# Optimization experiments

Hardware: AMD Instinct MI355X
Metric: run time of the kernel (lower is better)

The kernel has to match this reference:

```python
import jax, jax.numpy as jnp
import numpy as np

B = 4          # graphs
N = 8192       # coarse nodes (2048/graph)
M = 65536      # fine (skip) nodes (16384/graph)
E = 131072     # edges (32768/graph)
T = 16         # global tokens per graph
F_IN = 16      # dim of x and x_skip (concat -> in_channels = 32)
HID, OUT = 32, 16
ED, GD, EMB, H = 3, 1024, 64, 4
K = 3


def _make_pe(t, d):
    # PositionalEncoding buffer (sin/cos), deterministic constant
    position = np.arange(t, dtype=np.float32)[:, None]
    div = np.exp(np.arange(0, d, 2, dtype=np.float32) * (-np.log(10000.0) / d))
    pe = np.zeros((t, d), dtype=np.float32)
    pe[:, 0::2] = np.sin(position * div)
    pe[:, 1::2] = np.cos(position * div)
    return jnp.asarray(pe)


def setup_inputs():
    key = jax.random.key(0)
    ks = jax.random.split(key, 30)
    n, m, e = N // B, M // B, E // B
    inp = {}
    inp['x'] = jax.random.normal(ks[0], (N, F_IN), jnp.float32)
    inp['pos'] = jax.random.normal(ks[1], (N, 3), jnp.float32)
    inp['batch'] = jnp.repeat(jnp.arange(B), n)
    inp['x_skip'] = jax.random.normal(ks[2], (M, F_IN), jnp.float32)
    inp['pos_skip'] = jax.random.normal(ks[3], (M, 3), jnp.float32)
    inp['batch_skip'] = jnp.repeat(jnp.arange(B), m)
    off = jnp.repeat(jnp.arange(B) * m, e)
    inp['edge_index'] = jax.random.randint(ks[4], (2, E), 0, m) + off[None, :]
    inp['global_token'] = jax.random.normal(ks[5], (B * T, GD), jnp.float32)
    def lin(k, o, i, s):
        return jax.random.normal(k, (o, i), jnp.float32) * s
    inp['Wq_w'] = lin(ks[6], EMB, ED, 0.3); inp['Wq_b'] = jnp.zeros((EMB,), jnp.float32)
    inp['Wk_w'] = lin(ks[7], EMB, GD, 0.03); inp['Wk_b'] = jnp.zeros((EMB,), jnp.float32)
    inp['Wv_w'] = lin(ks[8], EMB, GD, 0.03); inp['Wv_b'] = jnp.zeros((EMB,), jnp.float32)
    inp['in_proj_w'] = lin(ks[9], 3 * EMB, EMB, 0.125); inp['in_proj_b'] = jnp.zeros((3 * EMB,), jnp.float32)
    inp['out_w'] = lin(ks[10], EMB, EMB, 0.125); inp['out_b'] = jnp.zeros((EMB,), jnp.float32)
    dims = [(2 * F_IN, HID), (HID, HID), (HID, OUT)]
    for i, (ci, co) in enumerate(dims):
        inp[f'nn_w{i}'] = lin(ks[11 + 3 * i], ci * co, ED + EMB, 0.05)
        inp[f'nn_b{i}'] = jnp.zeros((ci * co,), jnp.float32)
        inp[f'root{i}'] = jax.random.normal(ks[12 + 3 * i], (ci, co), jnp.float32) * (1.0 / np.sqrt(ci))
        inp[f'bias{i}'] = jnp.zeros((co,), jnp.float32)
    return inp


def reference(x, pos, batch, x_skip, pos_skip, batch_skip, edge_index, global_token,
              Wq_w, Wq_b, Wk_w, Wk_b, Wv_w, Wv_b, in_proj_w, in_proj_b, out_w, out_b,
              nn_w0, nn_b0, root0, bias0, nn_w1, nn_b1, root1, bias1, nn_w2, nn_b2, root2, bias2):
    # ---- knn_interpolate (k=3, inverse squared-distance weighting) ----
    # graphs are equal-sized by construction so per-graph knn == batched knn
    pos_b = pos.reshape(B, -1, 3)
    posk_b = pos_skip.reshape(B, -1, 3)
    d2 = ((posk_b ** 2).sum(-1)[:, :, None] + (pos_b ** 2).sum(-1)[:, None, :]
          - 2.0 * jnp.einsum('bmc,bnc->bmn', posk_b, pos_b))  # [B,m,n]
    neg, idx = jax.lax.top_k(-d2, K)                           # [B,m,K]
    w = 1.0 / jnp.maximum(-neg, 1e-16)
    x_b = x.reshape(B, -1, x.shape[-1])
    feats = jnp.take_along_axis(x_b[:, None, :, :], idx[:, :, :, None], axis=2)  # [B,m,K,F]
    xf = ((w[..., None] * feats).sum(2) / w.sum(2)[..., None]).reshape(M, -1)

    src, dst = edge_index[0], edge_index[1]
    pseudo = pos_skip[dst] - pos_skip[src]                     # patch_size is None
    edge_pos = (0.5 * (pos_skip[dst] + pos_skip[src])).reshape(B, -1, 3)
    gt = global_token.reshape(B, -1, global_token.shape[-1])
    pe = _make_pe(gt.shape[1], EMB)
    Q = edge_pos @ Wq_w.T + Wq_b                               # [B,Eb,EMB]
    Kt = gt @ Wk_w.T + Wk_b + pe                               # dropout in eval = identity
    Vt = gt @ Wv_w.T + Wv_b + pe
    # ---- MultiheadAttention (batch_first) ----
    wq, wk, wv = jnp.split(in_proj_w, 3, axis=0)
    bq, bk, bv = jnp.split(in_proj_b, 3, axis=0)
    hd = EMB // H
    def heads(t, w_, b_):
        t = t @ w_.T + b_
        return t.reshape(t.shape[0], t.shape[1], H, hd).transpose(0, 2, 1, 3)
    q, k_, v = heads(Q, wq, bq), heads(Kt, wk, bk), heads(Vt, wv, bv)
    att = jax.nn.softmax(jnp.einsum('bhqd,bhkd->bhqk', q, k_) / np.sqrt(hd).astype(np.float32), axis=-1)
    o = jnp.einsum('bhqk,bhkd->bhqd', att, v).transpose(0, 2, 1, 3).reshape(B, -1, EMB)
    o = o @ out_w.T + out_b
    pseudo = jnp.concatenate([pseudo, o.reshape(-1, EMB)], axis=-1)  # [E, 3+64]

    # ---- NNConv stack (gather -> edge MLP -> per-edge matmul -> scatter mean) ----
    h = jnp.concatenate([xf, x_skip], axis=1)                  # [M, 32]
    ones = jnp.ones((E,), jnp.float32)
    cnt = jnp.maximum(jax.ops.segment_sum(ones, dst, num_segments=M), 1.0)[:, None]
    for nw, nb, rt, bs in ((nn_w0, nn_b0, root0, bias0),
                           (nn_w1, nn_b1, root1, bias1),
                           (nn_w2, nn_b2, root2, bias2)):
        ci, co = rt.shape
        we = jax.nn.relu(pseudo @ nw.T + nb).reshape(E, ci, co)  # MLP (BN at default eval stats ~ identity)
        msg = jnp.einsum('ei,eio->eo', h[src], we)               # [E, co]
        aggr = jax.ops.segment_sum(msg, dst, num_segments=M) / cnt
        h = jax.nn.relu(aggr + h @ rt + bs)                      # drop_act=False -> relu every layer
    return h, pos_skip, batch_skip
```

## Files before the change

kernel.cpp:

```cpp
#include <hip/hip_runtime.h>
#include <math.h>

#define NB    4
#define NN    8192
#define MM    65536
#define EE    131072
#define NPG   2048

typedef short short8 __attribute__((ext_vector_type(8)));
typedef float f32x4  __attribute__((ext_vector_type(4)));

static __device__ inline unsigned short f2b(float f) {
    unsigned u = __float_as_uint(f);
    u += 0x7fffu + ((u >> 16) & 1u);
    return (unsigned short)(u >> 16);
}
static __device__ inline unsigned f2b_pack(float a, float b) {
    unsigned x = __float_as_uint(a); x += 0x7fffu + ((x >> 16) & 1u);
    unsigned y = __float_as_uint(b); y += 0x7fffu + ((y >> 16) & 1u);
    return (x >> 16) | (y & 0xffff0000u);
}
static __device__ inline short8 bc8(uint4 v) {
    union { uint4 u; short8 s; } c; c.u = v; return c.s;
}

__global__ __launch_bounds__(256)
void k_knn(const float* __restrict__ pos, const float* __restrict__ pos_skip,
           const float* __restrict__ x, const float* __restrict__ x_skip,
           const int* __restrict__ batch_skip,
           float* __restrict__ h0, float* __restrict__ out_pos,
           float* __restrict__ out_batch)
{
    __shared__ float4 cp[NPG];
    __shared__ unsigned pk[4][128][3];
    __shared__ float wFin[128][3];
    __shared__ int   iFin[128][3];

    int tid = threadIdx.x;
    int g = blockIdx.x >> 7;
    int cbase = g * NPG;
    for (int c = tid; c < NPG; c += 256) {
        float px = pos[(cbase + c) * 3 + 0];
        float py = pos[(cbase + c) * 3 + 1];
        float pz = pos[(cbase + c) * 3 + 2];
        cp[c] = make_float4(px, py, pz, px * px + py * py + pz * pz);
    }
    __syncthreads();

    int p = tid & 63;
    int slice = tid >> 6;
    int fbase = blockIdx.x * 128;
    int f0 = fbase + p, f1 = fbase + 64 + p;
    float fx0 = pos_skip[f0 * 3 + 0], fy0 = pos_skip[f0 * 3 + 1], fz0 = pos_skip[f0 * 3 + 2];
    float fx1 = pos_skip[f1 * 3 + 0], fy1 = pos_skip[f1 * 3 + 1], fz1 = pos_skip[f1 * 3 + 2];
    float fq0 = fx0 * fx0 + fy0 * fy0 + fz0 * fz0;
    float fq1 = fx1 * fx1 + fy1 * fy1 + fz1 * fz1;

    unsigned ka0 = 0xFFFFFFFFu, ka1 = 0xFFFFFFFFu, ka2 = 0xFFFFFFFFu;
    unsigned kb0 = 0xFFFFFFFFu, kb1 = 0xFFFFFFFFu, kb2 = 0xFFFFFFFFu;
    const float4* cps = cp + slice * 512;
#pragma unroll 8
    for (int l = 0; l < 512; ++l) {
        float4 cc = cps[l];
        float s0 = fx0 * cc.x + fy0 * cc.y + fz0 * cc.z;
        float d0 = fmaxf(fq0 + cc.w - 2.f * s0, 0.f);
        unsigned k = (__float_as_uint(d0) & 0xFFFFFE00u) | (unsigned)l;
        unsigned t1 = max(ka0, k); ka0 = min(ka0, k);
        unsigned t2 = max(ka1, t1); ka1 = min(ka1, t1);
        ka2 = min(ka2, t2);
        float s1 = fx1 * cc.x + fy1 * cc.y + fz1 * cc.z;
        float d1 = fmaxf(fq1 + cc.w - 2.f * s1, 0.f);
        unsigned kq = (__float_as_uint(d1) & 0xFFFFFE00u) | (unsigned)l;
        t1 = max(kb0, kq); kb0 = min(kb0, kq);
        t2 = max(kb1, t1); kb1 = min(kb1, t1);
        kb2 = min(kb2, t2);
    }
    pk[slice][p][0] = ka0; pk[slice][p][1] = ka1; pk[slice][p][2] = ka2;
    pk[slice][64 + p][0] = kb0; pk[slice][64 + p][1] = kb1; pk[slice][64 + p][2] = kb2;
    __syncthreads();

    if (tid < 128) {
        int n = tid;
        int f = fbase + n;
        float gx = pos_skip[f * 3 + 0], gy = pos_skip[f * 3 + 1], gz = pos_skip[f * 3 + 2];
        float gq = gx * gx + gy * gy + gz * gz;
        unsigned long long m0 = ~0ull, m1 = ~0ull, m2 = ~0ull;
#pragma unroll
        for (int s = 0; s < 4; ++s)
#pragma unroll
            for (int r = 0; r < 3; ++r) {
                unsigned key = pk[s][n][r];
                int c = s * 512 + (int)(key & 511u);
                float4 cc = cp[c];
                float d = fmaxf(gq + cc.w - 2.f * (gx * cc.x + gy * cc.y + gz * cc.z), 0.f);
                unsigned long long kk = ((unsigned long long)__float_as_uint(d) << 32) | (unsigned)c;
                unsigned long long t1 = m0 > kk ? m0 : kk; m0 = m0 < kk ? m0 : kk;
                unsigned long long t2 = m1 > t1 ? m1 : t1; m1 = m1 < t1 ? m1 : t1;
                m2 = m2 < t2 ? m2 : t2;
            }
        float d0 = __uint_as_float((unsigned)(m0 >> 32));
        float d1 = __uint_as_float((unsigned)(m1 >> 32));
        float d2 = __uint_as_float((unsigned)(m2 >> 32));
        float w0 = 1.f / fmaxf(d0, 1e-16f);
        float w1 = 1.f / fmaxf(d1, 1e-16f);
        float w2 = 1.f / fmaxf(d2, 1e-16f);
        float inv = 1.f / (w0 + w1 + w2);
        wFin[n][0] = w0 * inv; wFin[n][1] = w1 * inv; wFin[n][2] = w2 * inv;
        iFin[n][0] = cbase + (int)(m0 & 2047u);
        iFin[n][1] = cbase + (int)(m1 & 2047u);
        iFin[n][2] = cbase + (int)(m2 & 2047u);
        out_pos[f * 3 + 0] = gx; out_pos[f * 3 + 1] = gy; out_pos[f * 3 + 2] = gz;
        out_batch[f] = (float)batch_skip[f];
    }
    __syncthreads();

    int n2 = tid >> 1, half = tid & 1;
    int f2 = fbase + n2;
    float4* h04 = (float4*)(h0 + (size_t)f2 * 32);
    if (half == 0) {
        const float4* x4 = (const float4*)x;
        float w0 = wFin[n2][0], w1 = wFin[n2][1], w2 = wFin[n2][2];
        int a0 = iFin[n2][0] * 4, a1 = iFin[n2][1] * 4, a2 = iFin[n2][2] * 4;
#pragma unroll
        for (int j = 0; j < 4; ++j) {
            float4 v0 = x4[a0 + j], v1 = x4[a1 + j], v2 = x4[a2 + j];
            float4 r;
            r.x = w0 * v0.x + w1 * v1.x + w2 * v2.x;
            r.y = w0 * v0.y + w1 * v1.y + w2 * v2.y;
            r.z = w0 * v0.z + w1 * v1.z + w2 * v2.z;
            r.w = w0 * v0.w + w1 * v1.w + w2 * v2.w;
            h04[j] = r;
        }
    } else {
        const float4* xs4 = (const float4*)x_skip;
#pragma unroll
        for (int j = 0; j < 4; ++j) h04[4 + j] = xs4[f2 * 4 + j];
    }
}

__global__ __launch_bounds__(128)
void k_tokens1(const float* __restrict__ gt,
               const float* __restrict__ Wk_w, const float* __restrict__ Wk_b,
               const float* __restrict__ Wv_w, const float* __restrict__ Wv_b,
               float* __restrict__ KtVt)
{
    int b = blockIdx.x >> 4;
    int t = blockIdx.x & 15;
    int which = threadIdx.x >> 6;
    int d = threadIdx.x & 63;
    const float* W = which ? Wv_w : Wk_w;
    const float* bias = which ? Wv_b : Wk_b;
    const float4* row = (const float4*)(gt + (size_t)(b * 16 + t) * 1024);
    const float4* wr = (const float4*)(W + (size_t)d * 1024);
    float acc = 0.f;
    for (int c = 0; c < 256; ++c) {
        float4 a = row[c], w = wr[c];
        acc += a.x * w.x; acc += a.y * w.y; acc += a.z * w.z; acc += a.w * w.w;
    }
    int i2 = d >> 1;
    float dv = expf((float)(2 * i2) * (-0.14391156831212787f));
    float ang = (float)t * dv;
    float pe = (d & 1) ? cosf(ang) : sinf(ang);
    KtVt[((size_t)(b * 2 + which) * 16 + t) * 64 + d] = acc + bias[d] + pe;
}

__global__ __launch_bounds__(256)
void k_tokens2(const float* __restrict__ KtVt,
               const float* __restrict__ in_proj_w, const float* __restrict__ in_proj_b,
               const float* __restrict__ out_w,
               const float* __restrict__ Wq_w, const float* __restrict__ Wq_b,
               float* __restrict__ Mfold, uint4* __restrict__ v2fG)
{
    int b = blockIdx.x;
    int tid = threadIdx.x;
    __shared__ float KtL[1024], VtL[1024], vv[1024], kproj[1024];
    __shared__ float v2L[4096];
    __shared__ float qWs[192], qbs[64];
    for (int idx = tid; idx < 1024; idx += 256) {
        KtL[idx] = KtVt[(size_t)(b * 2 + 0) * 1024 + idx];
        VtL[idx] = KtVt[(size_t)(b * 2 + 1) * 1024 + idx];
    }
    __syncthreads();
    for (int idx = tid; idx < 2048; idx += 256) {
        int which = idx >> 10; int td = idx & 1023; int t = td >> 6; int j = td & 63;
        int r = (which ? 128 : 64) + j;
        const float* w = in_proj_w + (size_t)r * 64;
        const float* src = which ? VtL : KtL;
        float acc = in_proj_b[r];
#pragma unroll 8
        for (int dd = 0; dd < 64; ++dd) acc += src[t * 64 + dd] * w[dd];
        if (which) vv[t * 64 + j] = acc;
        else kproj[t * 64 + j] = acc;
    }
    for (int idx = tid; idx < 192; idx += 256) {
        int c = idx >> 6; int j = idx & 63;
        float acc = 0.f;
        for (int dd = 0; dd < 64; ++dd) acc += in_proj_w[(size_t)j * 64 + dd] * Wq_w[dd * 3 + c];
        qWs[c * 64 + j] = acc;
    }
    for (int j = tid; j < 64; j += 256) {
        float acc = in_proj_b[j];
        for (int dd = 0; dd < 64; ++dd) acc += in_proj_w[(size_t)j * 64 + dd] * Wq_b[dd];
        qbs[j] = acc;
    }
    __syncthreads();
    for (int idx = tid; idx < 4096; idx += 256) {
        int jo = idx & 63; int th2 = idx >> 6; int h = th2 & 3; int t = th2 >> 2;
        float acc = 0.f;
#pragma unroll
        for (int dd = 0; dd < 16; ++dd)
            acc += vv[t * 64 + h * 16 + dd] * out_w[(size_t)jo * 64 + h * 16 + dd];
        v2L[(t * 4 + h) * 64 + jo] = acc;
    }
    {
        int th = tid >> 2, c = tid & 3;
        int t = th >> 2, h = th & 3;
        float acc = 0.f;
#pragma unroll
        for (int dd = h * 16; dd < h * 16 + 16; ++dd) {
            float w = (c == 0) ? qWs[dd] : (c == 1) ? qWs[64 + dd]
                    : (c == 2) ? qWs[128 + dd] : qbs[dd];
            acc += w * kproj[t * 64 + dd];
        }
        Mfold[((size_t)b * 64 + th) * 4 + c] = 0.25f * acc;
    }
    __syncthreads();
    for (int it = tid; it < 512; it += 256) {
        int lane = it & 63, fi = it >> 6;
        int mi = fi >> 1, step = fi & 1;
        int outd = mi * 16 + (lane & 15);
        int th0 = step * 32 + (lane >> 4) * 8;
        uint4 v;
        v.x = f2b_pack(v2L[(th0 + 0) * 64 + outd], v2L[(th0 + 1) * 64 + outd]);
        v.y = f2b_pack(v2L[(th0 + 2) * 64 + outd], v2L[(th0 + 3) * 64 + outd]);
        v.z = f2b_pack(v2L[(th0 + 4) * 64 + outd], v2L[(th0 + 5) * 64 + outd]);
        v.w = f2b_pack(v2L[(th0 + 6) * 64 + outd], v2L[(th0 + 7) * 64 + outd]);
        v2fG[((size_t)b * 8 + fi) * 64 + lane] = v;
    }
}

__global__ __launch_bounds__(256)
void k_edge_attn(const float* __restrict__ ps, const int* __restrict__ ei,
                 const float* __restrict__ Mfold, const uint4* __restrict__ v2f,
                 const float* __restrict__ ob,
                 unsigned short* __restrict__ Pf, float* __restrict__ cnt)
{
    __shared__ unsigned attL[4 * 64 * 34];
    int tid = threadIdx.x;
    int wave = tid >> 6, lane = tid & 63, q = lane >> 4, c15 = lane & 15;
    int g = blockIdx.x >> 7;
    int e = blockIdx.x * 256 + tid;
    int s = ei[e], d = ei[EE + e];
    atomicAdd(&cnt[d], 1.f);
    float sx = ps[s * 3], sy = ps[s * 3 + 1], sz = ps[s * 3 + 2];
    float dx = ps[d * 3], dy = ps[d * 3 + 1], dz = ps[d * 3 + 2];
    float px = dx - sx, py = dy - sy, pz = dz - sz;
    float ex = 0.5f * (dx + sx), ey = 0.5f * (dy + sy), ez = 0.5f * (dz + sz);

    const float4* Mg = (const float4*)Mfold + (size_t)g * 64;
    float sc[64];
#pragma unroll
    for (int th = 0; th < 64; ++th) {
        float4 m = Mg[th];
        sc[th] = ex * m.x + ey * m.y + ez * m.z + m.w;
    }
#pragma unroll
    for (int h = 0; h < 4; ++h) {
        float mx = sc[h];
#pragma unroll
        for (int t = 1; t < 16; ++t) mx = fmaxf(mx, sc[t * 4 + h]);
        float ssum = 0.f;
#pragma unroll
        for (int t = 0; t < 16; ++t) {
            float eo = expf(sc[t * 4 + h] - mx);
            sc[t * 4 + h] = eo; ssum += eo;
        }
        float inv = 1.f / ssum;
#pragma unroll
        for (int t = 0; t < 16; ++t) sc[t * 4 + h] *= inv;
    }
    unsigned* slab = attL + wave * 64 * 34;
#pragma unroll
    for (int k = 0; k < 16; ++k) {
        uint2 v;
        v.x = f2b_pack(sc[4 * k + 0], sc[4 * k + 1]);
        v.y = f2b_pack(sc[4 * k + 2], sc[4 * k + 3]);
        *(uint2*)&slab[lane * 34 + 2 * k] = v;
    }
    __syncthreads();

    uint4 v2a[4][2];
#pragma unroll
    for (int mi = 0; mi < 4; ++mi)
#pragma unroll
        for (int st = 0; st < 2; ++st)
            v2a[mi][st] = v2f[((size_t)g * 8 + mi * 2 + st) * 64 + lane];

    f32x4 acc[4][4];
#pragma unroll
    for (int mi = 0; mi < 4; ++mi)
#pragma unroll
        for (int nt = 0; nt < 4; ++nt) acc[mi][nt] = (f32x4){0.f, 0.f, 0.f, 0.f};

#pragma unroll
    for (int nt = 0; nt < 4; ++nt) {
        const unsigned* rb = &slab[(nt * 16 + c15) * 34];
        uint4 b0 = *(const uint4*)&rb[q * 4];
        uint4 b1 = *(const uint4*)&rb[16 + q * 4];
#pragma unroll
        for (int mi = 0; mi < 4; ++mi) {
            acc[mi][nt] = __builtin_amdgcn_mfma_f32_16x16x32_bf16(bc8(v2a[mi][0]), bc8(b0), acc[mi][nt], 0, 0, 0);
            acc[mi][nt] = __builtin_amdgcn_mfma_f32_16x16x32_bf16(bc8(v2a[mi][1]), bc8(b1), acc[mi][nt], 0, 0, 0);
        }
    }
    __syncthreads();

    float4 obv[4];
#pragma unroll
    for (int mi = 0; mi < 4; ++mi) obv[mi] = *(const float4*)(ob + mi * 16 + q * 4);
#pragma unroll
    for (int mi = 0; mi < 4; ++mi)
#pragma unroll
        for (int nt = 0; nt < 4; ++nt) {
            f32x4 a = acc[mi][nt];
            uint2 v;
            v.x = f2b_pack(a[0] + obv[mi].x, a[1] + obv[mi].y);
            v.y = f2b_pack(a[2] + obv[mi].z, a[3] + obv[mi].w);
            *(uint2*)&slab[(nt * 16 + c15) * 34 + mi * 8 + q * 2] = v;
        }
    __syncthreads();

    uint4* Pf4 = (uint4*)Pf;
#pragma unroll
    for (int et = 0; et < 4; ++et) {
        int etg = blockIdx.x * 16 + wave * 4 + et;
#pragma unroll
        for (int st = 0; st < 2; ++st) {
            uint4 w = *(const uint4*)&slab[(et * 16 + c15) * 34 + st * 16 + q * 4];
            Pf4[((size_t)etg * 3 + st) * 64 + lane] = w;
        }
    }
    int et2 = e >> 4, eL = e & 15;
    size_t tb = ((size_t)(et2 * 3 + 2) * 64 + 0 * 16 + eL) * 8;
    uint2 t0; t0.x = f2b_pack(px, py); t0.y = f2b_pack(pz, 1.0f);
    *(uint2*)(Pf + tb) = t0;
    uint2 z2; z2.x = 0u; z2.y = 0u;
    *(uint2*)(Pf + tb + 4) = z2;
#pragma unroll
    for (int quad = 1; quad < 4; ++quad) {
        size_t zb = ((size_t)(et2 * 3 + 2) * 64 + quad * 16 + eL) * 8;
        uint4 z4; z4.x = 0u; z4.y = 0u; z4.z = 0u; z4.w = 0u;
        *(uint4*)(Pf + zb) = z4;
    }
}

static __device__ inline void repack_one(const float* __restrict__ nw,
                                         const float* __restrict__ nb,
                                         unsigned short* __restrict__ Wf, int idx)
{
    int jj = idx & 7;
    int lane = (idx >> 3) & 63;
    int rest = idx >> 9;
    int s = rest % 3;
    int jt = rest / 3;
    int j = jt * 16 + (lane & 15);
    int k = s * 32 + (lane >> 4) * 8 + jj;
    float v;
    if (k < 64)       v = nw[(size_t)j * 67 + 3 + k];
    else if (k < 67)  v = nw[(size_t)j * 67 + (k - 64)];
    else if (k == 67) v = nb[j];
    else              v = 0.f;
    Wf[idx] = f2b(v);
}

__global__ __launch_bounds__(256)
void k_repackAll(const float* __restrict__ nw0, const float* __restrict__ nb0,
                 const float* __restrict__ nw1, const float* __restrict__ nb1,
                 const float* __restrict__ nw2, const float* __restrict__ nb2,
                 unsigned short* __restrict__ Wf0, unsigned short* __restrict__ Wf1,
                 unsigned short* __restrict__ Wf2)
{
    int idx = blockIdx.x * 256 + threadIdx.x;
    if (idx < 98304)        repack_one(nw0, nb0, Wf0, idx);
    else if (idx < 196608)  repack_one(nw1, nb1, Wf1, idx - 98304);
    else                    repack_one(nw2, nb2, Wf2, idx - 196608);
}

template<int CO>
__global__ __launch_bounds__(256, 4)
void k_conv_mfma(const uint4* __restrict__ Pf, const float* __restrict__ hin,
                 const int* __restrict__ ei, const uint4* __restrict__ Wf,
                 float* __restrict__ aggr)
{
    constexpr int JT = 2 * CO;
    constexpr int NPAR = CO / 16;
    __shared__ float hL[128 * 36];
    __shared__ int sL[128];
    __shared__ int dL[128];

    int tid = threadIdx.x;
    int e0 = blockIdx.x * 128;
    if (tid < 128) sL[tid] = ei[e0 + tid];
    else           dL[tid - 128] = ei[EE + e0 + (tid - 128)];
    __syncthreads();
    for (int idx = tid; idx < 1024; idx += 256) {
        int row = idx >> 3, c = idx & 7;
        const float4* hr = (const float4*)(hin + (size_t)sL[row] * 32);
        *(float4*)&hL[row * 36 + c * 4] = hr[c];
    }
    __syncthreads();

    int wave = tid >> 6, lane = tid & 63, quad = lane >> 4, col = lane & 15;

    uint4 a[2][3];
    int et0 = blockIdx.x * 8 + wave * 2;
#pragma unroll
    for (int st = 0; st < 2; ++st)
#pragma unroll
        for (int s = 0; s < 3; ++s)
            a[st][s] = Pf[((size_t)(et0 + st) * 3 + s) * 64 + lane];

    float msg[2][NPAR][4];
#pragma unroll
    for (int st = 0; st < 2; ++st)
#pragma unroll
        for (int p = 0; p < NPAR; ++p)
#pragma unroll
            for (int r = 0; r < 4; ++r) msg[st][p][r] = 0.f;

#pragma unroll 2
    for (int jt = 0; jt < JT; ++jt) {
        uint4 b0 = Wf[((size_t)jt * 3 + 0) * 64 + lane];
        uint4 b1 = Wf[((size_t)jt * 3 + 1) * 64 + lane];
        uint4 b2 = Wf[((size_t)jt * 3 + 2) * 64 + lane];
        int i   = (CO == 32) ? (jt >> 1) : jt;
        int par = (CO == 32) ? (jt & 1) : 0;
#pragma unroll
        for (int st = 0; st < 2; ++st) {
            f32x4 c = {0.f, 0.f, 0.f, 0.f};
            c = __builtin_amdgcn_mfma_f32_16x16x32_bf16(bc8(a[st][0]), bc8(b0), c, 0, 0, 0);
            c = __builtin_amdgcn_mfma_f32_16x16x32_bf16(bc8(a[st][1]), bc8(b1), c, 0, 0, 0);
            c = __builtin_amdgcn_mfma_f32_16x16x32_bf16(bc8(a[st][2]), bc8(b2), c, 0, 0, 0);
#pragma unroll
            for (int r = 0; r < 4; ++r) {
                float hv = hL[(wave * 32 + st * 16 + quad * 4 + r) * 36 + i];
                msg[st][par][r] += hv * fmaxf(c[r], 0.f);
            }
        }
    }

#pragma unroll
    for (int st = 0; st < 2; ++st)
#pragma unroll
        for (int r = 0; r < 4; ++r) {
            int dv = dL[wave * 32 + st * 16 + quad * 4 + r];
#pragma unroll
            for (int p = 0; p < NPAR; ++p)
                atomicAdd(&aggr[(size_t)dv * CO + p * 16 + col], msg[st][p][r]);
        }
}

template<int CO>
__global__ __launch_bounds__(256)
void k_update(float* __restrict__ aggr, const float* __restrict__ cnt,
              const float* __restrict__ hin, const float* __restrict__ root,
              const float* __restrict__ bias, float* __restrict__ hout)
{
    __shared__ float rL[32 * CO];
    __shared__ float bL[CO];
    int tid = threadIdx.x;
    for (int idx = tid; idx < 32 * CO; idx += 256) rL[idx] = root[idx];
    if (tid < CO) bL[tid] = bias[tid];
    __syncthreads();
    int gid = blockIdx.x * 256 + tid;
    int v = gid / CO;
    int o = gid % CO;
    float acc = aggr[gid] / fmaxf(cnt[v], 1.f) + bL[o];
    aggr[gid] = 0.f;
    const float* hr = hin + (size_t)v * 32;
#pragma unroll
    for (int i = 0; i < 32; ++i) acc += hr[i] * rL[i * CO + o];
    hout[gid] = fmaxf(acc, 0.f);
}

extern "C" void kernel_launch(void* const* d_in, const int* in_sizes, int n_in,
                              void* d_out, int out_size, void* d_ws, size_t ws_size,
                              hipStream_t stream)
{
    const float* x          = (const float*)d_in[0];
    const float* pos        = (const float*)d_in[1];
    const float* x_skip     = (const float*)d_in[3];
    const float* pos_skip   = (const float*)d_in[4];
    const int*   batch_skip = (const int*)  d_in[5];
    const int*   ei         = (const int*)  d_in[6];
    const float* gt         = (const float*)d_in[7];
    const float* Wq_w       = (const float*)d_in[8];
    const float* Wq_b       = (const float*)d_in[9];
    const float* Wk_w       = (const float*)d_in[10];
    const float* Wk_b       = (const float*)d_in[11];
    const float* Wv_w       = (const float*)d_in[12];
    const float* Wv_b       = (const float*)d_in[13];
    const float* in_proj_w  = (const float*)d_in[14];
    const float* in_proj_b  = (const float*)d_in[15];
    const float* out_w      = (const float*)d_in[16];
    const float* out_b      = (const float*)d_in[17];
    const float* nn_w0 = (const float*)d_in[18]; const float* nn_b0 = (const float*)d_in[19];
    const float* root0 = (const float*)d_in[20]; const float* bias0 = (const float*)d_in[21];
    const float* nn_w1 = (const float*)d_in[22]; const float* nn_b1 = (const float*)d_in[23];
    const float* root1 = (const float*)d_in[24]; const float* bias1 = (const float*)d_in[25];
    const float* nn_w2 = (const float*)d_in[26]; const float* nn_b2 = (const float*)d_in[27];
    const float* root2 = (const float*)d_in[28]; const float* bias2 = (const float*)d_in[29];

    char* wsb = (char*)d_ws;
    size_t off = 0;
    auto carve = [&](size_t bytes) { char* p = wsb + off; off += (bytes + 255) & ~(size_t)255; return p; };
    float* aggr = (float*)carve((size_t)MM * 32 * 4);
    float* cnt  = (float*)carve((size_t)MM * 4);
    float* hA   = (float*)carve((size_t)MM * 32 * 4);
    float* hB   = (float*)carve((size_t)MM * 32 * 4);
    unsigned short* Pf  = (unsigned short*)carve((size_t)EE * 96 * 2);
    unsigned short* Wf0 = (unsigned short*)carve((size_t)1024 * 96 * 2);
    unsigned short* Wf1 = (unsigned short*)carve((size_t)1024 * 96 * 2);
    unsigned short* Wf2 = (unsigned short*)carve((size_t)512 * 96 * 2);
    float* Mfold = (float*)carve((size_t)NB * 64 * 4 * 4);
    uint4* v2f   = (uint4*)carve((size_t)NB * 8 * 64 * 16);
    float* KtVt  = (float*)carve((size_t)NB * 2 * 16 * 64 * 4);

    float* h_final   = (float*)d_out;
    float* out_pos   = (float*)d_out + (size_t)MM * 16;
    float* out_batch = (float*)d_out + (size_t)MM * 19;

    hipMemsetAsync(aggr, 0, ((size_t)MM * 32 + MM) * sizeof(float), stream);

    k_tokens1<<<64, 128, 0, stream>>>(gt, Wk_w, Wk_b, Wv_w, Wv_b, KtVt);
    k_tokens2<<<NB, 256, 0, stream>>>(KtVt, in_proj_w, in_proj_b, out_w, Wq_w, Wq_b,
                                      Mfold, v2f);
    k_knn<<<MM / 128, 256, 0, stream>>>(pos, pos_skip, x, x_skip, batch_skip,
                                        hA, out_pos, out_batch);
    k_edge_attn<<<EE / 256, 256, 0, stream>>>(pos_skip, ei, Mfold, v2f, out_b,
                                              Pf, cnt);
    k_repackAll<<<960, 256, 0, stream>>>(nn_w0, nn_b0, nn_w1, nn_b1, nn_w2, nn_b2,
                                         Wf0, Wf1, Wf2);

    k_conv_mfma<32><<<EE / 128, 256, 0, stream>>>((const uint4*)Pf, hA, ei, (const uint4*)Wf0, aggr);
    k_update<32><<<(MM * 32) / 256, 256, 0, stream>>>(aggr, cnt, hA, root0, bias0, hB);
    k_conv_mfma<32><<<EE / 128, 256, 0, stream>>>((const uint4*)Pf, hB, ei, (const uint4*)Wf1, aggr);
    k_update<32><<<(MM * 32) / 256, 256, 0, stream>>>(aggr, cnt, hB, root1, bias1, hA);
    k_conv_mfma<16><<<EE / 128, 256, 0, stream>>>((const uint4*)Pf, hA, ei, (const uint4*)Wf2, aggr);
    k_update<16><<<(MM * 16) / 256, 256, 0, stream>>>(aggr, cnt, hA, root2, bias2, h_final);
}
```

Baseline: 388.8 us.

## Restructure kNN to one node per thread and double edges per conv block

The kNN kernel now handles 64 fine nodes per block instead of 128, one per thread. It folds the -2 factor into the cached coarse positions, uses an FMA chain for distances, and keeps the top-3 as floats updated with fmed3. The NNConv MFMA kernel now processes 256 edges per block (4 MFMA tiles per wave) and loops over input channels with the h values hoisted, so each weight fragment load is reused across twice as many edges. Launch bounds drop to 2 blocks per CU to make room for the extra registers and shared memory, which may reduce occupancy and halves the number of conv blocks.

```diff
diff --git a/kernel.cpp b/kernel.cpp
--- a/kernel.cpp
+++ b/kernel.cpp
@@ -32,67 +32,64 @@
            float* __restrict__ out_batch)
 {
     __shared__ float4 cp[NPG];
-    __shared__ unsigned pk[4][128][3];
-    __shared__ float wFin[128][3];
-    __shared__ int   iFin[128][3];
+    __shared__ float  pk[4][64][3];
+    __shared__ float  wFin[64][3];
+    __shared__ int    iFin[64][3];
 
     int tid = threadIdx.x;
-    int g = blockIdx.x >> 7;
+    int g = blockIdx.x >> 8;
     int cbase = g * NPG;
     for (int c = tid; c < NPG; c += 256) {
         float px = pos[(cbase + c) * 3 + 0];
         float py = pos[(cbase + c) * 3 + 1];
         float pz = pos[(cbase + c) * 3 + 2];
-        cp[c] = make_float4(px, py, pz, px * px + py * py + pz * pz);
-    }
-    __syncthreads();
-
-    int p = tid & 63;
+        cp[c] = make_float4(-2.f * px, -2.f * py, -2.f * pz, px * px + py * py + pz * pz);
+    }
+    __syncthreads();
+
+    int node = tid & 63;
     int slice = tid >> 6;
-    int fbase = blockIdx.x * 128;
-    int f0 = fbase + p, f1 = fbase + 64 + p;
-    float fx0 = pos_skip[f0 * 3 + 0], fy0 = pos_skip[f0 * 3 + 1], fz0 = pos_skip[f0 * 3 + 2];
-    float fx1 = pos_skip[f1 * 3 + 0], fy1 = pos_skip[f1 * 3 + 1], fz1 = pos_skip[f1 * 3 + 2];
-    float fq0 = fx0 * fx0 + fy0 * fy0 + fz0 * fz0;
-    float fq1 = fx1 * fx1 + fy1 * fy1 + fz1 * fz1;
-
-    unsigned ka0 = 0xFFFFFFFFu, ka1 = 0xFFFFFFFFu, ka2 = 0xFFFFFFFFu;
-    unsigned kb0 = 0xFFFFFFFFu, kb1 = 0xFFFFFFFFu, kb2 = 0xFFFFFFFFu;
+    int fbase = blockIdx.x * 64;
+    int f = fbase + node;
+    float fx = pos_skip[f * 3 + 0], fy = pos_skip[f * 3 + 1], fz = pos_skip[f * 3 + 2];
+    float fqe = fx * fx + fy * fy + fz * fz + 1e-5f;
+
+    float k0 = 3.4028235e38f, k1 = 3.4028235e38f, k2 = 3.4028235e38f;
     const float4* cps = cp + slice * 512;
 #pragma unroll 8
     for (int l = 0; l < 512; ++l) {
         float4 cc = cps[l];
-        float s0 = fx0 * cc.x + fy0 * cc.y + fz0 * cc.z;
-        float d0 = fmaxf(fq0 + cc.w - 2.f * s0, 0.f);
-        unsigned k = (__float_as_uint(d0) & 0xFFFFFE00u) | (unsigned)l;
-        unsigned t1 = max(ka0, k); ka0 = min(ka0, k);
-        unsigned t2 = max(ka1, t1); ka1 = min(ka1, t1);
-        ka2 = min(ka2, t2);
-        float s1 = fx1 * cc.x + fy1 * cc.y + fz1 * cc.z;
-        float d1 = fmaxf(fq1 + cc.w - 2.f * s1, 0.f);
-        unsigned kq = (__float_as_uint(d1) & 0xFFFFFE00u) | (unsigned)l;
-        t1 = max(kb0, kq); kb0 = min(kb0, kq);
-        t2 = max(kb1, t1); kb1 = min(kb1, t1);
-        kb2 = min(kb2, t2);
-    }
-    pk[slice][p][0] = ka0; pk[slice][p][1] = ka1; pk[slice][p][2] = ka2;
-    pk[slice][64 + p][0] = kb0; pk[slice][64 + p][1] = kb1; pk[slice][64 + p][2] = kb2;
-    __syncthreads();
-
-    if (tid < 128) {
+        float d = fqe + cc.w;
+        d = fmaf(cc.x, fx, d);
+        d = fmaf(cc.y, fy, d);
+        d = fmaf(cc.z, fz, d);
+        float key = __uint_as_float((__float_as_uint(d) & 0xFFFFFE00u) | (unsigned)l);
+        float t = fmaxf(k1, key);
+        k2 = fminf(k2, t);
+        k1 = __builtin_amdgcn_fmed3f(k0, k1, key);
+        k0 = fminf(k0, key);
+    }
+    pk[slice][node][0] = k0; pk[slice][node][1] = k1; pk[slice][node][2] = k2;
+    __syncthreads();
+
+    if (tid < 64) {
         int n = tid;
-        int f = fbase + n;
-        float gx = pos_skip[f * 3 + 0], gy = pos_skip[f * 3 + 1], gz = pos_skip[f * 3 + 2];
+        int fn = fbase + n;
+        float gx = pos_skip[fn * 3 + 0], gy = pos_skip[fn * 3 + 1], gz = pos_skip[fn * 3 + 2];
         float gq = gx * gx + gy * gy + gz * gz;
         unsigned long long m0 = ~0ull, m1 = ~0ull, m2 = ~0ull;
 #pragma unroll
         for (int s = 0; s < 4; ++s)
 #pragma unroll
             for (int r = 0; r < 3; ++r) {
-                unsigned key = pk[s][n][r];
+                unsigned key = __float_as_uint(pk[s][n][r]);
                 int c = s * 512 + (int)(key & 511u);
                 float4 cc = cp[c];
-                float d = fmaxf(gq + cc.w - 2.f * (gx * cc.x + gy * cc.y + gz * cc.z), 0.f);
+                float d = gq + cc.w;
+                d = fmaf(cc.x, gx, d);
+                d = fmaf(cc.y, gy, d);
+                d = fmaf(cc.z, gz, d);
+                d = fmaxf(d, 0.f);
                 unsigned long long kk = ((unsigned long long)__float_as_uint(d) << 32) | (unsigned)c;
                 unsigned long long t1 = m0 > kk ? m0 : kk; m0 = m0 < kk ? m0 : kk;
                 unsigned long long t2 = m1 > t1 ? m1 : t1; m1 = m1 < t1 ? m1 : t1;
@@ -109,32 +106,36 @@
         iFin[n][0] = cbase + (int)(m0 & 2047u);
         iFin[n][1] = cbase + (int)(m1 & 2047u);
         iFin[n][2] = cbase + (int)(m2 & 2047u);
-        out_pos[f * 3 + 0] = gx; out_pos[f * 3 + 1] = gy; out_pos[f * 3 + 2] = gz;
-        out_batch[f] = (float)batch_skip[f];
-    }
-    __syncthreads();
-
-    int n2 = tid >> 1, half = tid & 1;
+        out_pos[fn * 3 + 0] = gx; out_pos[fn * 3 + 1] = gy; out_pos[fn * 3 + 2] = gz;
+        out_batch[fn] = (float)batch_skip[fn];
+    }
+    __syncthreads();
+
+    int n2 = tid >> 2, part = tid & 3;
     int f2 = fbase + n2;
     float4* h04 = (float4*)(h0 + (size_t)f2 * 32);
-    if (half == 0) {
+    if (part < 2) {
         const float4* x4 = (const float4*)x;
         float w0 = wFin[n2][0], w1 = wFin[n2][1], w2 = wFin[n2][2];
         int a0 = iFin[n2][0] * 4, a1 = iFin[n2][1] * 4, a2 = iFin[n2][2] * 4;
 #pragma unroll
-        for (int j = 0; j < 4; ++j) {
-            float4 v0 = x4[a0 + j], v1 = x4[a1 + j], v2 = x4[a2 + j];
+        for (int j = 0; j < 2; ++j) {
+            int cj = part * 2 + j;
+            float4 v0 = x4[a0 + cj], v1 = x4[a1 + cj], v2 = x4[a2 + cj];
             float4 r;
             r.x = w0 * v0.x + w1 * v1.x + w2 * v2.x;
             r.y = w0 * v0.y + w1 * v1.y + w2 * v2.y;
             r.z = w0 * v0.z + w1 * v1.z + w2 * v2.z;
             r.w = w0 * v0.w + w1 * v1.w + w2 * v2.w;
-            h04[j] = r;
+            h04[cj] = r;
         }
     } else {
         const float4* xs4 = (const float4*)x_skip;
 #pragma unroll
-        for (int j = 0; j < 4; ++j) h04[4 + j] = xs4[f2 * 4 + j];
+        for (int j = 0; j < 2; ++j) {
+            int cj = (part - 2) * 2 + j;
+            h04[4 + cj] = xs4[f2 * 4 + cj];
+        }
     }
 }
 
@@ -387,23 +388,22 @@
 }
 
 template<int CO>
-__global__ __launch_bounds__(256, 4)
+__global__ __launch_bounds__(256, 2)
 void k_conv_mfma(const uint4* __restrict__ Pf, const float* __restrict__ hin,
                  const int* __restrict__ ei, const uint4* __restrict__ Wf,
                  float* __restrict__ aggr)
 {
-    constexpr int JT = 2 * CO;
     constexpr int NPAR = CO / 16;
-    __shared__ float hL[128 * 36];
-    __shared__ int sL[128];
-    __shared__ int dL[128];
+    __shared__ float hL[256 * 36];
+    __shared__ int sL[256];
+    __shared__ int dL[256];
 
     int tid = threadIdx.x;
-    int e0 = blockIdx.x * 128;
-    if (tid < 128) sL[tid] = ei[e0 + tid];
-    else           dL[tid - 128] = ei[EE + e0 + (tid - 128)];
-    __syncthreads();
-    for (int idx = tid; idx < 1024; idx += 256) {
+    int e0 = blockIdx.x * 256;
+    sL[tid] = ei[e0 + tid];
+    dL[tid] = ei[EE + e0 + tid];
+    __syncthreads();
+    for (int idx = tid; idx < 2048; idx += 256) {
         int row = idx >> 3, c = idx & 7;
         const float4* hr = (const float4*)(hin + (size_t)sL[row] * 32);
         *(float4*)&hL[row * 36 + c * 4] = hr[c];
@@ -412,48 +412,54 @@
 
     int wave = tid >> 6, lane = tid & 63, quad = lane >> 4, col = lane & 15;
 
-    uint4 a[2][3];
-    int et0 = blockIdx.x * 8 + wave * 2;
-#pragma unroll
-    for (int st = 0; st < 2; ++st)
+    uint4 a[4][3];
+    int et0 = blockIdx.x * 16 + wave * 4;
+#pragma unroll
+    for (int st = 0; st < 4; ++st)
 #pragma unroll
         for (int s = 0; s < 3; ++s)
             a[st][s] = Pf[((size_t)(et0 + st) * 3 + s) * 64 + lane];
 
-    float msg[2][NPAR][4];
-#pragma unroll
-    for (int st = 0; st < 2; ++st)
+    float msg[4][NPAR][4];
+#pragma unroll
+    for (int st = 0; st < 4; ++st)
 #pragma unroll
         for (int p = 0; p < NPAR; ++p)
 #pragma unroll
             for (int r = 0; r < 4; ++r) msg[st][p][r] = 0.f;
 
-#pragma unroll 2
-    for (int jt = 0; jt < JT; ++jt) {
-        uint4 b0 = Wf[((size_t)jt * 3 + 0) * 64 + lane];
-        uint4 b1 = Wf[((size_t)jt * 3 + 1) * 64 + lane];
-        uint4 b2 = Wf[((size_t)jt * 3 + 2) * 64 + lane];
-        int i   = (CO == 32) ? (jt >> 1) : jt;
-        int par = (CO == 32) ? (jt & 1) : 0;
-#pragma unroll
-        for (int st = 0; st < 2; ++st) {
-            f32x4 c = {0.f, 0.f, 0.f, 0.f};
-            c = __builtin_amdgcn_mfma_f32_16x16x32_bf16(bc8(a[st][0]), bc8(b0), c, 0, 0, 0);
-            c = __builtin_amdgcn_mfma_f32_16x16x32_bf16(bc8(a[st][1]), bc8(b1), c, 0, 0, 0);
-            c = __builtin_amdgcn_mfma_f32_16x16x32_bf16(bc8(a[st][2]), bc8(b2), c, 0, 0, 0);
-#pragma unroll
-            for (int r = 0; r < 4; ++r) {
-                float hv = hL[(wave * 32 + st * 16 + quad * 4 + r) * 36 + i];
-                msg[st][par][r] += hv * fmaxf(c[r], 0.f);
+    for (int i = 0; i < 32; ++i) {
+        if (CO == 16 && i >= 32) break;
+        float hv[4][4];
+#pragma unroll
+        for (int st = 0; st < 4; ++st)
+#pragma unroll
+            for (int r = 0; r < 4; ++r)
+                hv[st][r] = hL[(wave * 64 + st * 16 + quad * 4 + r) * 36 + i];
+#pragma unroll
+        for (int par = 0; par < NPAR; ++par) {
+            int jt = (CO == 32) ? (i * 2 + par) : i;
+            uint4 b0 = Wf[((size_t)jt * 3 + 0) * 64 + lane];
+            uint4 b1 = Wf[((size_t)jt * 3 + 1) * 64 + lane];
+            uint4 b2 = Wf[((size_t)jt * 3 + 2) * 64 + lane];
+#pragma unroll
+            for (int st = 0; st < 4; ++st) {
+                f32x4 c = {0.f, 0.f, 0.f, 0.f};
+                c = __builtin_amdgcn_mfma_f32_16x16x32_bf16(bc8(a[st][0]), bc8(b0), c, 0, 0, 0);
+                c = __builtin_amdgcn_mfma_f32_16x16x32_bf16(bc8(a[st][1]), bc8(b1), c, 0, 0, 0);
+                c = __builtin_amdgcn_mfma_f32_16x16x32_bf16(bc8(a[st][2]), bc8(b2), c, 0, 0, 0);
+#pragma unroll
+                for (int r = 0; r < 4; ++r)
+                    msg[st][par][r] += hv[st][r] * fmaxf(c[r], 0.f);
             }
         }
     }
 
 #pragma unroll
-    for (int st = 0; st < 2; ++st)
+    for (int st = 0; st < 4; ++st)
 #pragma unroll
         for (int r = 0; r < 4; ++r) {
-            int dv = dL[wave * 32 + st * 16 + quad * 4 + r];
+            int dv = dL[wave * 64 + st * 16 + quad * 4 + r];
 #pragma unroll
             for (int p = 0; p < NPAR; ++p)
                 atomicAdd(&aggr[(size_t)dv * CO + p * 16 + col], msg[st][p][r]);
@@ -535,17 +541,17 @@
     k_tokens1<<<64, 128, 0, stream>>>(gt, Wk_w, Wk_b, Wv_w, Wv_b, KtVt);
     k_tokens2<<<NB, 256, 0, stream>>>(KtVt, in_proj_w, in_proj_b, out_w, Wq_w, Wq_b,
                                       Mfold, v2f);
-    k_knn<<<MM / 128, 256, 0, stream>>>(pos, pos_skip, x, x_skip, batch_skip,
-                                        hA, out_pos, out_batch);
+    k_knn<<<MM / 64, 256, 0, stream>>>(pos, pos_skip, x, x_skip, batch_skip,
+                                       hA, out_pos, out_batch);
     k_edge_attn<<<EE / 256, 256, 0, stream>>>(pos_skip, ei, Mfold, v2f, out_b,
                                               Pf, cnt);
     k_repackAll<<<960, 256, 0, stream>>>(nn_w0, nn_b0, nn_w1, nn_b1, nn_w2, nn_b2,
                                          Wf0, Wf1, Wf2);
 
-    k_conv_mfma<32><<<EE / 128, 256, 0, stream>>>((const uint4*)Pf, hA, ei, (const uint4*)Wf0, aggr);
+    k_conv_mfma<32><<<EE / 256, 256, 0, stream>>>((const uint4*)Pf, hA, ei, (const uint4*)Wf0, aggr);
     k_update<32><<<(MM * 32) / 256, 256, 0, stream>>>(aggr, cnt, hA, root0, bias0, hB);
-    k_conv_mfma<32><<<EE / 128, 256, 0, stream>>>((const uint4*)Pf, hB, ei, (const uint4*)Wf1, aggr);
+    k_conv_mfma<32><<<EE / 256, 256, 0, stream>>>((const uint4*)Pf, hB, ei, (const uint4*)Wf1, aggr);
     k_update<32><<<(MM * 32) / 256, 256, 0, stream>>>(aggr, cnt, hB, root1, bias1, hA);
-    k_conv_mfma<16><<<EE / 128, 256, 0, stream>>>((const uint4*)Pf, hA, ei, (const uint4*)Wf2, aggr);
+    k_conv_mfma<16><<<EE / 256, 256, 0, stream>>>((const uint4*)Pf, hA, ei, (const uint4*)Wf2, aggr);
     k_update<16><<<(MM * 16) / 256, 256, 0, stream>>>(aggr, cnt, hA, root2, bias2, h_final);
 }
```

After: 390.8 us. Within noise of the previous version (+0.5%).
